# Optimization experiments

Measured on AMD Instinct MI355X. Metric: run time of the kernel, lower is better.

The kernel has to match this reference:

```python
import jax, jax.numpy as jnp
import numpy as np

N = 10000
E = 160000
B = 16
NEG_SLOPE = 0.2


def gat_conv(x, src, dst, W, a_src, a_dst, b, heads, ch):
    # x: [N, F_in]; src/dst: [E'] (self-loops included); W: [F_in, heads*ch]
    n = x.shape[0]
    h = (x @ W).reshape(n, heads, ch)                     # [N,H,C]
    alpha_src = jnp.sum(h * a_src, axis=-1)               # [N,H]
    alpha_dst = jnp.sum(h * a_dst, axis=-1)               # [N,H]
    e = jax.nn.leaky_relu(alpha_src[src] + alpha_dst[dst], NEG_SLOPE)  # [E,H]
    # segment softmax over edges grouped by destination node
    m = jax.ops.segment_max(e, dst, num_segments=n)       # [N,H]
    ex = jnp.exp(e - m[dst])                              # [E,H]
    denom = jax.ops.segment_sum(ex, dst, num_segments=n)  # [N,H]
    alpha = ex / denom[dst]                               # [E,H]
    out = jax.ops.segment_sum(alpha[:, :, None] * h[src], dst, num_segments=n)  # [N,H,C]
    return out.reshape(n, heads * ch) + b


def setup_inputs() -> dict:
    key = jax.random.key(0)
    ks = jax.random.split(key, 16)
    glorot = lambda k, shp: jax.random.normal(k, shp, jnp.float32) * np.sqrt(2.0 / (shp[0] + shp[-1]))
    inp = {
        "x": jax.random.normal(ks[0], (N, 128), jnp.float32),
        "edge_index": jax.random.randint(ks[1], (2, E), 0, N, jnp.int64),
        "batch": jnp.sort(jax.random.randint(ks[2], (N,), 0, B, jnp.int64)),
        # conv1: 128 -> 128 per head, 8 heads
        "W1": glorot(ks[3], (128, 8 * 128)),
        "att_src1": glorot(ks[4], (8, 128)),
        "att_dst1": glorot(ks[5], (8, 128)),
        "b1": jnp.zeros((8 * 128,), jnp.float32),
        # conv2: 1024 -> 64 per head, 8 heads
        "W2": glorot(ks[6], (1024, 8 * 64)),
        "att_src2": glorot(ks[7], (8, 64)),
        "att_dst2": glorot(ks[8], (8, 64)),
        "b2": jnp.zeros((8 * 64,), jnp.float32),
        "fc1_w": glorot(ks[9], (512, 32)),
        "fc1_b": jnp.zeros((32,), jnp.float32),
        "fc2_w": glorot(ks[10], (32, 10)),
        "fc2_b": jnp.zeros((10,), jnp.float32),
    }
    return inp


def reference(x, edge_index, batch, W1, att_src1, att_dst1, b1,
              W2, att_src2, att_dst2, b2, fc1_w, fc1_b, fc2_w, fc2_b):
    n = x.shape[0]
    loop = jnp.arange(n, dtype=edge_index.dtype)
    src = jnp.concatenate([edge_index[0], loop])  # PyG add_self_loops=True
    dst = jnp.concatenate([edge_index[1], loop])
    h = jax.nn.elu(gat_conv(x, src, dst, W1, att_src1, att_dst1, b1, 8, 128))   # [N,1024]
    h = jax.nn.elu(gat_conv(h, src, dst, W2, att_src2, att_dst2, b2, 8, 64))    # [N,512]
    # global mean pool over graphs
    sums = jax.ops.segment_sum(h, batch, num_segments=B)                        # [B,512]
    cnt = jax.ops.segment_sum(jnp.ones((n,), h.dtype), batch, num_segments=B)
    g = sums / jnp.maximum(cnt, 1.0)[:, None]
    g = jax.nn.elu(g @ fc1_w + fc1_b)
    return g @ fc2_w + fc2_b                                                    # [B,10]
```

## Files before the change

kernel.cpp:

```cpp
#include <hip/hip_runtime.h>
#include <math.h>

#define HEADS 8
#define NEG 0.2f

typedef unsigned short ushort_t;
typedef __attribute__((ext_vector_type(8))) short short8;
typedef float f32x4 __attribute__((ext_vector_type(4)));

__device__ inline ushort_t f2bf(float f) {
  union { float f; unsigned u; } v; v.f = f;
  unsigned r = (v.u + 0x7FFF + ((v.u >> 16) & 1)) >> 16;
  return (ushort_t)r;
}

__device__ inline float4 bf4(uint2 v) {
  union { unsigned u; float f; } a, b, c, d;
  a.u = v.x << 16; b.u = v.x & 0xffff0000u;
  c.u = v.y << 16; d.u = v.y & 0xffff0000u;
  return make_float4(a.f, b.f, c.f, d.f);
}

__device__ inline float elu_f(float v) {
  return (v > 0.f) ? v : (__expf(v) - 1.f);
}

#define GLDS16(gp, lp)                                                          \
  __builtin_amdgcn_global_load_lds(                                             \
      (const __attribute__((address_space(1))) void*)(gp),                      \
      (__attribute__((address_space(3))) void*)(lp), 16, 0, 0)

__global__ __launch_bounds__(256) void init_k(int* __restrict__ ws, int zero_words,
                                              const float* __restrict__ x,
                                              ushort_t* __restrict__ xb,
                                              const float* __restrict__ W1,
                                              ushort_t* __restrict__ w1t,
                                              const float* __restrict__ W2,
                                              ushort_t* __restrict__ w2t, int nx4) {
  __shared__ float tile[32][33];
  int blk = blockIdx.x;
  if (blk < 640) {
    const float* W; ushort_t* Wt; int K, N, tk, tn;
    if (blk < 128) { W = W1; Wt = w1t; K = 128; N = 1024; tk = blk >> 5; tn = blk & 31; }
    else { W = W2; Wt = w2t; K = 1024; N = 512; int t = blk - 128; tk = t >> 4; tn = t & 15; }
    int tx = threadIdx.x & 31, ty = threadIdx.x >> 5;
    int k0 = tk * 32, n0 = tn * 32;
#pragma unroll
    for (int r = 0; r < 4; r++)
      tile[ty + r * 8][tx] = W[(size_t)(k0 + ty + r * 8) * N + n0 + tx];
    __syncthreads();
#pragma unroll
    for (int r = 0; r < 4; r++)
      Wt[(size_t)(n0 + ty + r * 8) * K + k0 + tx] = f2bf(tile[tx][ty + r * 8]);
  } else {
    int i = (blk - 640) * 256 + threadIdx.x;
    if (i < zero_words) ws[i] = 0;
    if (i < nx4) {
      float4 v = ((const float4*)x)[i];
      ushort_t o[4] = {f2bf(v.x), f2bf(v.y), f2bf(v.z), f2bf(v.w)};
      *(uint2*)&xb[i * 4] = *(uint2*)o;
    }
  }
}

__global__ void prep_k(const int* __restrict__ ei, int* __restrict__ src,
                       int* __restrict__ dst, int* __restrict__ deg,
                       const int* __restrict__ batch, int* __restrict__ bstart,
                       int* __restrict__ bend, int E, int Nn) {
  int i = blockIdx.x * blockDim.x + threadIdx.x;
  if (i < Nn) {
    int b = batch[i];
    if (i == 0 || batch[i - 1] != b) bstart[b] = i;
    if (i == Nn - 1 || batch[i + 1] != b) bend[b] = i + 1;
  }
  if (i >= E + Nn) return;
  int s, d;
  if (i < E) { s = ei[i]; d = ei[E + i]; }
  else       { s = d = i - E; }
  src[i] = s;
  dst[i] = d;
  atomicAdd(&deg[d], 1);
}

__global__ __launch_bounds__(1024) void scan_k(const int* __restrict__ deg,
                                               int* __restrict__ offs,
                                               int* __restrict__ cursor, int Nn) {
  __shared__ int wtot[16];
  __shared__ int wexcl[16];
  __shared__ int soff_s;
  int t = threadIdx.x;
  int lane = t & 63, w = t >> 6;
  if (t == 0) soff_s = 0;
  __syncthreads();
  for (int base = 0; base < Nn; base += 4096) {
    int idx = base + 4 * t;
    int4 v = make_int4(0, 0, 0, 0);
    if (idx + 3 < Nn) v = *(const int4*)&deg[idx];
    else {
      if (idx < Nn)     v.x = deg[idx];
      if (idx + 1 < Nn) v.y = deg[idx + 1];
      if (idx + 2 < Nn) v.z = deg[idx + 2];
      if (idx + 3 < Nn) v.w = deg[idx + 3];
    }
    int s1 = v.x, s2 = s1 + v.y, s3 = s2 + v.z, s4 = s3 + v.w;
    int sc = s4;
#pragma unroll
    for (int o = 1; o < 64; o <<= 1) {
      int x = __shfl_up(sc, o);
      if (lane >= o) sc += x;
    }
    if (lane == 63) wtot[w] = sc;
    __syncthreads();
    if (w == 0) {
      int tv = (lane < 16) ? wtot[lane] : 0;
      int ts = tv;
#pragma unroll
      for (int o = 1; o < 16; o <<= 1) {
        int x = __shfl_up(ts, o);
        if (lane >= o) ts += x;
      }
      if (lane < 16) wexcl[lane] = ts - tv;
      if (lane == 15) wtot[15] = ts;
    }
    __syncthreads();
    int excl = soff_s + wexcl[w] + (sc - s4);
    int o0 = excl, o1 = excl + s1, o2 = excl + s2, o3 = excl + s3;
    if (idx < Nn)     { offs[idx] = o0;     cursor[idx] = o0; }
    if (idx + 1 < Nn) { offs[idx + 1] = o1; cursor[idx + 1] = o1; }
    if (idx + 2 < Nn) { offs[idx + 2] = o2; cursor[idx + 2] = o2; }
    if (idx + 3 < Nn) { offs[idx + 3] = o3; cursor[idx + 3] = o3; }
    int chunk_total = wtot[15];
    __syncthreads();
    if (t == 0) soff_s += chunk_total;
    __syncthreads();
  }
  if (t == 0) offs[Nn] = soff_s;
}

__global__ void scatter_k(const int* __restrict__ src, const int* __restrict__ dst,
                          int* __restrict__ cursor, int* __restrict__ psrc, int Etot) {
  int i = blockIdx.x * blockDim.x + threadIdx.x;
  if (i >= Etot) return;
  int p = atomicAdd(&cursor[dst[i]], 1);
  psrc[p] = src[i];
}

__global__ __launch_bounds__(256) void mfma_gemm_k(const ushort_t* __restrict__ A,
                                                   const ushort_t* __restrict__ Bt,
                                                   ushort_t* __restrict__ Cb,
                                                   const float* __restrict__ att_s,
                                                   const float* __restrict__ att_d,
                                                   float* __restrict__ asrc,
                                                   float* __restrict__ adst,
                                                   int M, int N, int K, int CSHIFT) {
  __shared__ __attribute__((aligned(16))) ushort_t As[128 * 64];
  __shared__ __attribute__((aligned(16))) ushort_t Bs[128 * 64];
  int tid = threadIdx.x;
  int lane = tid & 63;
  int wave = tid >> 6;
  int wm = (wave >> 1) * 64, wn = (wave & 1) * 64;
  int bm = blockIdx.y * 128, bn = blockIdx.x * 128;
  int lrow = lane & 15, lq = lane >> 4;

  f32x4 acc[4][4];
#pragma unroll
  for (int i = 0; i < 4; i++)
#pragma unroll
    for (int j = 0; j < 4; j++) acc[i][j] = 0.f;

  int srow = lane >> 3;
  int scol = 8 * ((lane & 7) ^ srow);
  const ushort_t* pa[4];
  const ushort_t* pb[4];
  ushort_t* la[4];
  ushort_t* lb[4];
#pragma unroll
  for (int c = 0; c < 4; c++) {
    int row = wave * 32 + c * 8 + srow;
    int ga = min(bm + row, M - 1);
    pa[c] = &A[(size_t)ga * K + scol];
    pb[c] = &Bt[(size_t)(bn + row) * K + scol];
    la[c] = &As[(wave * 4 + c) * 512];
    lb[c] = &Bs[(wave * 4 + c) * 512];
  }

  for (int k0 = 0; k0 < K; k0 += 64) {
    __syncthreads();
#pragma unroll
    for (int c = 0; c < 4; c++) GLDS16(pa[c] + k0, la[c]);
#pragma unroll
    for (int c = 0; c < 4; c++) GLDS16(pb[c] + k0, lb[c]);
    __syncthreads();
#pragma unroll
    for (int ks = 0; ks < 2; ks++) {
      short8 af[4], bfr[4];
#pragma unroll
      for (int t = 0; t < 4; t++) {
        int cbs = (ks * 64 + lq * 16) ^ ((lrow & 7) << 4);
        af[t]  = *(const short8*)&As[(wm + t * 16 + lrow) * 64 + (cbs >> 1)];
        bfr[t] = *(const short8*)&Bs[(wn + t * 16 + lrow) * 64 + (cbs >> 1)];
      }
#pragma unroll
      for (int i = 0; i < 4; i++)
#pragma unroll
        for (int j = 0; j < 4; j++)
          acc[i][j] = __builtin_amdgcn_mfma_f32_16x16x32_bf16(af[i], bfr[j], acc[i][j], 0, 0, 0);
    }
  }

  {
    int hh = (bn + wn) >> CSHIFT;
    float avs[4], avd[4];
#pragma unroll
    for (int j = 0; j < 4; j++) {
      int col = bn + wn + j * 16 + lrow;
      avs[j] = att_s[col];
      avd[j] = att_d[col];
    }
#pragma unroll
    for (int i = 0; i < 4; i++) {
#pragma unroll
      for (int r = 0; r < 4; r++) {
        float ps = 0.f, pd = 0.f;
#pragma unroll
        for (int j = 0; j < 4; j++) {
          float v = acc[i][j][r];
          ps += v * avs[j];
          pd += v * avd[j];
        }
#pragma unroll
        for (int o = 1; o < 16; o <<= 1) {
          ps += __shfl_xor(ps, o);
          pd += __shfl_xor(pd, o);
        }
        int row = bm + wm + i * 16 + lq * 4 + r;
        if (lrow == 0 && row < M) {
          atomicAdd(&asrc[row * HEADS + hh], ps);
          atomicAdd(&adst[row * HEADS + hh], pd);
        }
      }
    }
  }

#pragma unroll
  for (int i = 0; i < 4; i++) {
    int row0 = bm + wm + i * 16 + lq * 4;
#pragma unroll
    for (int j = 0; j < 4; j++) {
      int col = bn + wn + j * 16 + lrow;
#pragma unroll
      for (int r = 0; r < 4; r++) {
        int row = row0 + r;
        if (row < M) Cb[(size_t)row * N + col] = f2bf(acc[i][j][r]);
      }
    }
  }
}

template <int F, int CSHIFT, int BT, int NSPLIT, typename OT>
__global__ __launch_bounds__(BT) void aggregate_k(const ushort_t* __restrict__ hb,
                                                  const float* __restrict__ asrc,
                                                  const float* __restrict__ adst,
                                                  const int* __restrict__ offs,
                                                  const int* __restrict__ psrc,
                                                  const float* __restrict__ bias,
                                                  OT* __restrict__ out) {
  constexpr int CPB = F / NSPLIT;
  static_assert(CPB == 4 * BT, "CPB/thread mismatch");
  int nb = blockIdx.x;
  int n = nb / NSPLIT;
  int coff = (nb - n * NSPLIT) * CPB;
  int t = threadIdx.x;
  int c0 = coff + 4 * t;
  int hh = c0 >> CSHIFT;
  float adn = adst[n * HEADS + hh];
  int e0 = offs[n], e1 = offs[n + 1];
  float4 acc = make_float4(0.f, 0.f, 0.f, 0.f);
  float wsum = 0.f;

  int i = e0;
  int s[8];
  if (i + 8 <= e1) {
#pragma unroll
    for (int u = 0; u < 8; u++) s[u] = psrc[i + u];
  }
  while (i + 8 <= e1) {
    uint2 r[8];
    float av[8];
#pragma unroll
    for (int u = 0; u < 8; u++) r[u] = *(const uint2*)&hb[(size_t)s[u] * F + c0];
#pragma unroll
    for (int u = 0; u < 8; u++) av[u] = asrc[s[u] * HEADS + hh];
    i += 8;
    bool more = (i + 8 <= e1);
    int sn[8];
#pragma unroll
    for (int u = 0; u < 8; u++) sn[u] = more ? psrc[i + u] : 0;
#pragma unroll
    for (int u = 0; u < 8; u++) {
      float v = av[u] + adn;
      v = (v > 0.f) ? v : NEG * v;
      float w = __expf(v);
      float4 f = bf4(r[u]);
      wsum += w;
      acc.x += w * f.x;
      acc.y += w * f.y;
      acc.z += w * f.z;
      acc.w += w * f.w;
    }
#pragma unroll
    for (int u = 0; u < 8; u++) s[u] = sn[u];
  }
  for (; i < e1; i++) {
    int ss = psrc[i];
    float v = asrc[ss * HEADS + hh] + adn;
    v = (v > 0.f) ? v : NEG * v;
    float w = __expf(v);
    float4 f = bf4(*(const uint2*)&hb[(size_t)ss * F + c0]);
    wsum += w;
    acc.x += w * f.x; acc.y += w * f.y;
    acc.z += w * f.z; acc.w += w * f.w;
  }

  float inv = 1.f / wsum;
  float v0 = elu_f(acc.x * inv + bias[c0]);
  float v1 = elu_f(acc.y * inv + bias[c0 + 1]);
  float v2 = elu_f(acc.z * inv + bias[c0 + 2]);
  float v3 = elu_f(acc.w * inv + bias[c0 + 3]);
  if (sizeof(OT) == 2) {
    unsigned p0 = (unsigned)f2bf(v0) | ((unsigned)f2bf(v1) << 16);
    unsigned p1 = (unsigned)f2bf(v2) | ((unsigned)f2bf(v3) << 16);
    *(uint2*)&((ushort_t*)out)[(size_t)n * F + c0] = make_uint2(p0, p1);
  } else {
    *(float4*)&((float*)out)[(size_t)n * F + c0] = make_float4(v0, v1, v2, v3);
  }
}

__global__ __launch_bounds__(256) void pool_k(const float* __restrict__ g,
                                              const int* __restrict__ batch,
                                              float* __restrict__ sums, int Nn) {
  int c = blockIdx.x * 256 + threadIdx.x;
  int n0 = blockIdx.y * 50;
  int n1 = min(n0 + 50, Nn);
  if (n0 >= n1) return;
  float acc = 0.f;
  int cur = batch[n0];
  for (int n = n0; n < n1; n++) {
    int b = batch[n];
    if (b != cur) { atomicAdd(&sums[cur * 512 + c], acc); acc = 0.f; cur = b; }
    acc += g[(size_t)n * 512 + c];
  }
  atomicAdd(&sums[cur * 512 + c], acc);
}

__global__ __launch_bounds__(512) void mlp_k(const float* __restrict__ sums,
                                             const int* __restrict__ bstart,
                                             const int* __restrict__ bend,
                                             const float* __restrict__ w1,
                                             const float* __restrict__ b1,
                                             const float* __restrict__ w2,
                                             const float* __restrict__ b2,
                                             float* __restrict__ out) {
  __shared__ float gm[16 * 512];
  __shared__ float t1[16 * 32];
  int t = threadIdx.x;
  for (int i = t; i < 16 * 512; i += 512) {
    int b = i >> 9;
    float c = (float)(bend[b] - bstart[b]);
    gm[i] = sums[i] / fmaxf(c, 1.f);
  }
  __syncthreads();
  {
    int b = t >> 5, j = t & 31;
    float s = b1[j];
    for (int k = 0; k < 512; k++) s += gm[(b << 9) + k] * w1[k * 32 + j];
    t1[t] = elu_f(s);
  }
  __syncthreads();
  if (t < 160) {
    int b = t / 10, j = t - b * 10;
    float s = b2[j];
#pragma unroll
    for (int k = 0; k < 32; k++) s += t1[b * 32 + k] * w2[k * 10 + j];
    out[t] = s;
  }
}

extern "C" void kernel_launch(void* const* d_in, const int* in_sizes, int n_in,
                              void* d_out, int out_size, void* d_ws, size_t ws_size,
                              hipStream_t stream) {
  const float* x   = (const float*)d_in[0];
  const int*   ei  = (const int*)d_in[1];
  const int* batch = (const int*)d_in[2];
  const float* W1  = (const float*)d_in[3];
  const float* as1 = (const float*)d_in[4];
  const float* ad1 = (const float*)d_in[5];
  const float* b1  = (const float*)d_in[6];
  const float* W2  = (const float*)d_in[7];
  const float* as2 = (const float*)d_in[8];
  const float* ad2 = (const float*)d_in[9];
  const float* b2  = (const float*)d_in[10];
  const float* f1w = (const float*)d_in[11];
  const float* f1b = (const float*)d_in[12];
  const float* f2w = (const float*)d_in[13];
  const float* f2b = (const float*)d_in[14];
  float* out = (float*)d_out;

  const int Nn = in_sizes[2];
  const int E = in_sizes[1] / 2;
  const int Etot = E + Nn;

  size_t off = 0;
  auto alloc = [&](size_t elems) { size_t o = off; off += (elems + 63) & ~(size_t)63; return o; };
  int* wsi = (int*)d_ws;
  float* wsf = (float*)d_ws;

  size_t o_deg  = alloc(Nn);
  size_t o_pool = alloc(16 * 512);
  size_t o_as1  = alloc((size_t)Nn * 8);
  size_t o_ad1  = alloc((size_t)Nn * 8);
  size_t o_as2  = alloc((size_t)Nn * 8);
  size_t o_ad2  = alloc((size_t)Nn * 8);
  size_t zero_words = off;
  size_t o_bst  = alloc(64);
  size_t o_ben  = alloc(64);
  size_t o_offs = alloc(Nn + 1);
  size_t o_cur  = alloc(Nn);
  size_t o_src  = alloc(Etot);
  size_t o_dst  = alloc(Etot);
  size_t o_psrc = alloc(Etot);
  size_t o_xb   = alloc((size_t)Nn * 128 / 2);
  size_t o_w1t  = alloc(1024 * 128 / 2);
  size_t o_w2t  = alloc(512 * 1024 / 2);
  size_t o_h    = alloc((size_t)Nn * 1024 / 2);
  size_t o_g    = alloc((size_t)Nn * 1024);

  ushort_t* xb  = (ushort_t*)(wsi + o_xb);
  ushort_t* w1t = (ushort_t*)(wsi + o_w1t);
  ushort_t* w2t = (ushort_t*)(wsi + o_w2t);
  ushort_t* hb  = (ushort_t*)(wsi + o_h);
  ushort_t* g1b = (ushort_t*)(wsi + o_g);

  int eb = (Etot + 255) / 256;

  int nx4 = Nn * 128 / 4;
  int ep_work = (int)((zero_words > (size_t)nx4 ? zero_words : (size_t)nx4));
  int init_blocks = 640 + (ep_work + 255) / 256;
  init_k<<<init_blocks, 256, 0, stream>>>(wsi, (int)zero_words, x, xb,
                                          W1, w1t, W2, w2t, nx4);
  prep_k<<<eb, 256, 0, stream>>>(ei, wsi + o_src, wsi + o_dst, wsi + o_deg,
                                 batch, wsi + o_bst, wsi + o_ben, E, Nn);
  scan_k<<<1, 1024, 0, stream>>>(wsi + o_deg, wsi + o_offs, wsi + o_cur, Nn);
  scatter_k<<<eb, 256, 0, stream>>>(wsi + o_src, wsi + o_dst, wsi + o_cur,
                                    wsi + o_psrc, Etot);

  mfma_gemm_k<<<dim3(1024 / 128, (Nn + 127) / 128), 256, 0, stream>>>(
      xb, w1t, hb, as1, ad1, wsf + o_as1, wsf + o_ad1, Nn, 1024, 128, 7);
  aggregate_k<1024, 7, 128, 2, ushort_t><<<Nn * 2, 128, 0, stream>>>(
      hb, wsf + o_as1, wsf + o_ad1, wsi + o_offs, wsi + o_psrc, b1, g1b);

  mfma_gemm_k<<<dim3(512 / 128, (Nn + 127) / 128), 256, 0, stream>>>(
      g1b, w2t, hb, as2, ad2, wsf + o_as2, wsf + o_ad2, Nn, 512, 1024, 6);
  aggregate_k<512, 6, 64, 2, float><<<Nn * 2, 64, 0, stream>>>(
      hb, wsf + o_as2, wsf + o_ad2, wsi + o_offs, wsi + o_psrc, b2, wsf + o_g);

  pool_k<<<dim3(2, (Nn + 49) / 50), 256, 0, stream>>>(wsf + o_g, batch, wsf + o_pool, Nn);
  mlp_k<<<1, 512, 0, stream>>>(wsf + o_pool, wsi + o_bst, wsi + o_ben, f1w, f1b, f2w, f2b, out);
}
```

Before: 276.4 us.

## Precompute per-edge attention weights in a separate kernel before aggregation

Adds a weights_k kernel that computes exp(leaky_relu(asrc+adst)) once per edge and head, stored head-major in a workspace buffer. scatter_k now also writes the CSR-sorted destination index so this kernel can run. The aggregate kernels then read precomputed weights instead of gathering asrc and recomputing exp in every thread that shares a head. This removes redundant exp and gather work in the aggregation, at the cost of two extra launches, an extra pdst array and a write plus read of an E×8 float buffer per layer.

New measurement: 287.3 us. 3.9% more time.

```diff
diff --git a/kernel.cpp b/kernel.cpp
--- a/kernel.cpp
+++ b/kernel.cpp
@@ -138,11 +138,36 @@
 }
 
 __global__ void scatter_k(const int* __restrict__ src, const int* __restrict__ dst,
-                          int* __restrict__ cursor, int* __restrict__ psrc, int Etot) {
+                          int* __restrict__ cursor, int* __restrict__ psrc,
+                          int* __restrict__ pdst, int Etot) {
   int i = blockIdx.x * blockDim.x + threadIdx.x;
   if (i >= Etot) return;
-  int p = atomicAdd(&cursor[dst[i]], 1);
+  int d = dst[i];
+  int p = atomicAdd(&cursor[d], 1);
   psrc[p] = src[i];
+  pdst[p] = d;
+}
+
+__global__ __launch_bounds__(256) void weights_k(const int* __restrict__ psrc,
+                                                 const int* __restrict__ pdst,
+                                                 const float* __restrict__ asrc,
+                                                 const float* __restrict__ adst,
+                                                 float* __restrict__ w, int Etot) {
+  int p = blockIdx.x * 256 + threadIdx.x;
+  if (p >= Etot) return;
+  int s = psrc[p], d = pdst[p];
+  const float4* sa = (const float4*)&asrc[(size_t)s * 8];
+  const float4* da = (const float4*)&adst[(size_t)d * 8];
+  float4 s0 = sa[0], s1 = sa[1];
+  float4 d0 = da[0], d1 = da[1];
+  float vv[8] = {s0.x + d0.x, s0.y + d0.y, s0.z + d0.z, s0.w + d0.w,
+                 s1.x + d1.x, s1.y + d1.y, s1.z + d1.z, s1.w + d1.w};
+#pragma unroll
+  for (int h = 0; h < 8; h++) {
+    float v = vv[h];
+    v = (v > 0.f) ? v : NEG * v;
+    w[(size_t)h * Etot + p] = __expf(v);
+  }
 }
 
 __global__ __launch_bounds__(256) void mfma_gemm_k(const ushort_t* __restrict__ A,
@@ -259,12 +284,11 @@
 
 template <int F, int CSHIFT, int BT, int NSPLIT, typename OT>
 __global__ __launch_bounds__(BT) void aggregate_k(const ushort_t* __restrict__ hb,
-                                                  const float* __restrict__ asrc,
-                                                  const float* __restrict__ adst,
+                                                  const float* __restrict__ w,
                                                   const int* __restrict__ offs,
                                                   const int* __restrict__ psrc,
                                                   const float* __restrict__ bias,
-                                                  OT* __restrict__ out) {
+                                                  OT* __restrict__ out, int Etot) {
   constexpr int CPB = F / NSPLIT;
   static_assert(CPB == 4 * BT, "CPB/thread mismatch");
   int nb = blockIdx.x;
@@ -273,53 +297,52 @@
   int t = threadIdx.x;
   int c0 = coff + 4 * t;
   int hh = c0 >> CSHIFT;
-  float adn = adst[n * HEADS + hh];
+  const float* __restrict__ wp = w + (size_t)hh * Etot;
   int e0 = offs[n], e1 = offs[n + 1];
   float4 acc = make_float4(0.f, 0.f, 0.f, 0.f);
   float wsum = 0.f;
 
   int i = e0;
   int s[8];
+  float wv[8];
   if (i + 8 <= e1) {
 #pragma unroll
     for (int u = 0; u < 8; u++) s[u] = psrc[i + u];
+#pragma unroll
+    for (int u = 0; u < 8; u++) wv[u] = wp[i + u];
   }
   while (i + 8 <= e1) {
     uint2 r[8];
-    float av[8];
 #pragma unroll
     for (int u = 0; u < 8; u++) r[u] = *(const uint2*)&hb[(size_t)s[u] * F + c0];
-#pragma unroll
-    for (int u = 0; u < 8; u++) av[u] = asrc[s[u] * HEADS + hh];
     i += 8;
     bool more = (i + 8 <= e1);
     int sn[8];
+    float wn[8];
 #pragma unroll
     for (int u = 0; u < 8; u++) sn[u] = more ? psrc[i + u] : 0;
 #pragma unroll
+    for (int u = 0; u < 8; u++) wn[u] = more ? wp[i + u] : 0.f;
+#pragma unroll
     for (int u = 0; u < 8; u++) {
-      float v = av[u] + adn;
-      v = (v > 0.f) ? v : NEG * v;
-      float w = __expf(v);
+      float wt = wv[u];
       float4 f = bf4(r[u]);
-      wsum += w;
-      acc.x += w * f.x;
-      acc.y += w * f.y;
-      acc.z += w * f.z;
-      acc.w += w * f.w;
-    }
-#pragma unroll
-    for (int u = 0; u < 8; u++) s[u] = sn[u];
+      wsum += wt;
+      acc.x += wt * f.x;
+      acc.y += wt * f.y;
+      acc.z += wt * f.z;
+      acc.w += wt * f.w;
+    }
+#pragma unroll
+    for (int u = 0; u < 8; u++) { s[u] = sn[u]; wv[u] = wn[u]; }
   }
   for (; i < e1; i++) {
     int ss = psrc[i];
-    float v = asrc[ss * HEADS + hh] + adn;
-    v = (v > 0.f) ? v : NEG * v;
-    float w = __expf(v);
+    float wt = wp[i];
     float4 f = bf4(*(const uint2*)&hb[(size_t)ss * F + c0]);
-    wsum += w;
-    acc.x += w * f.x; acc.y += w * f.y;
-    acc.z += w * f.z; acc.w += w * f.w;
+    wsum += wt;
+    acc.x += wt * f.x; acc.y += wt * f.y;
+    acc.z += wt * f.z; acc.w += wt * f.w;
   }
 
   float inv = 1.f / wsum;
@@ -429,6 +452,8 @@
   size_t o_src  = alloc(Etot);
   size_t o_dst  = alloc(Etot);
   size_t o_psrc = alloc(Etot);
+  size_t o_pdst = alloc(Etot);
+  size_t o_w    = alloc((size_t)Etot * 8);
   size_t o_xb   = alloc((size_t)Nn * 128 / 2);
   size_t o_w1t  = alloc(1024 * 128 / 2);
   size_t o_w2t  = alloc(512 * 1024 / 2);
@@ -452,17 +477,21 @@
                                  batch, wsi + o_bst, wsi + o_ben, E, Nn);
   scan_k<<<1, 1024, 0, stream>>>(wsi + o_deg, wsi + o_offs, wsi + o_cur, Nn);
   scatter_k<<<eb, 256, 0, stream>>>(wsi + o_src, wsi + o_dst, wsi + o_cur,
-                                    wsi + o_psrc, Etot);
+                                    wsi + o_psrc, wsi + o_pdst, Etot);
 
   mfma_gemm_k<<<dim3(1024 / 128, (Nn + 127) / 128), 256, 0, stream>>>(
       xb, w1t, hb, as1, ad1, wsf + o_as1, wsf + o_ad1, Nn, 1024, 128, 7);
+  weights_k<<<eb, 256, 0, stream>>>(wsi + o_psrc, wsi + o_pdst,
+                                    wsf + o_as1, wsf + o_ad1, wsf + o_w, Etot);
   aggregate_k<1024, 7, 128, 2, ushort_t><<<Nn * 2, 128, 0, stream>>>(
-      hb, wsf + o_as1, wsf + o_ad1, wsi + o_offs, wsi + o_psrc, b1, g1b);
+      hb, wsf + o_w, wsi + o_offs, wsi + o_psrc, b1, g1b, Etot);
 
   mfma_gemm_k<<<dim3(512 / 128, (Nn + 127) / 128), 256, 0, stream>>>(
       g1b, w2t, hb, as2, ad2, wsf + o_as2, wsf + o_ad2, Nn, 512, 1024, 6);
+  weights_k<<<eb, 256, 0, stream>>>(wsi + o_psrc, wsi + o_pdst,
+                                    wsf + o_as2, wsf + o_ad2, wsf + o_w, Etot);
   aggregate_k<512, 6, 64, 2, float><<<Nn * 2, 64, 0, stream>>>(
-      hb, wsf + o_as2, wsf + o_ad2, wsi + o_offs, wsi + o_psrc, b2, wsf + o_g);
+      hb, wsf + o_w, wsi + o_offs, wsi + o_psrc, b2, wsf + o_g, Etot);
 
   pool_k<<<dim3(2, (Nn + 49) / 50), 256, 0, stream>>>(wsf + o_g, batch, wsf + o_pool, Nn);
   mlp_k<<<1, 512, 0, stream>>>(wsf + o_pool, wsi + o_bst, wsi + o_ben, f1w, f1b, f2w, f2b, out);
```

## Double-buffer LDS tiles in MFMA GEMM to overlap global loads with compute

Applied to the files above, without the earlier changes.

Doubles the shared-memory A/B tiles and restructures the K loop so the next tile is staged via direct global-to-LDS loads while MFMAs run on the current buffer. A single waitcnt plus barrier per iteration replaces the two __syncthreads. This is meant to hide global load latency behind compute. In exchange, LDS use doubles to 64KB per block, which may reduce occupancy.

Result: no change. 279.4 us (+1.1%).

```diff
diff --git a/kernel.cpp b/kernel.cpp
--- a/kernel.cpp
+++ b/kernel.cpp
@@ -153,8 +153,8 @@
                                                    float* __restrict__ asrc,
                                                    float* __restrict__ adst,
                                                    int M, int N, int K, int CSHIFT) {
-  __shared__ __attribute__((aligned(16))) ushort_t As[128 * 64];
-  __shared__ __attribute__((aligned(16))) ushort_t Bs[128 * 64];
+  __shared__ __attribute__((aligned(16))) ushort_t As[2][128 * 64];
+  __shared__ __attribute__((aligned(16))) ushort_t Bs[2][128 * 64];
   int tid = threadIdx.x;
   int lane = tid & 63;
   int wave = tid >> 6;
@@ -172,33 +172,32 @@
   int scol = 8 * ((lane & 7) ^ srow);
   const ushort_t* pa[4];
   const ushort_t* pb[4];
-  ushort_t* la[4];
-  ushort_t* lb[4];
+  int lofs[4];
 #pragma unroll
   for (int c = 0; c < 4; c++) {
     int row = wave * 32 + c * 8 + srow;
     int ga = min(bm + row, M - 1);
     pa[c] = &A[(size_t)ga * K + scol];
     pb[c] = &Bt[(size_t)(bn + row) * K + scol];
-    la[c] = &As[(wave * 4 + c) * 512];
-    lb[c] = &Bs[(wave * 4 + c) * 512];
-  }
-
-  for (int k0 = 0; k0 < K; k0 += 64) {
-    __syncthreads();
-#pragma unroll
-    for (int c = 0; c < 4; c++) GLDS16(pa[c] + k0, la[c]);
-#pragma unroll
-    for (int c = 0; c < 4; c++) GLDS16(pb[c] + k0, lb[c]);
-    __syncthreads();
+    lofs[c] = (wave * 4 + c) * 512;
+  }
+
+  auto stage = [&](int buf, int k0) {
+#pragma unroll
+    for (int c = 0; c < 4; c++) GLDS16(pa[c] + k0, &As[buf][lofs[c]]);
+#pragma unroll
+    for (int c = 0; c < 4; c++) GLDS16(pb[c] + k0, &Bs[buf][lofs[c]]);
+  };
+
+  auto compute = [&](int buf) {
 #pragma unroll
     for (int ks = 0; ks < 2; ks++) {
       short8 af[4], bfr[4];
 #pragma unroll
       for (int t = 0; t < 4; t++) {
         int cbs = (ks * 64 + lq * 16) ^ ((lrow & 7) << 4);
-        af[t]  = *(const short8*)&As[(wm + t * 16 + lrow) * 64 + (cbs >> 1)];
-        bfr[t] = *(const short8*)&Bs[(wn + t * 16 + lrow) * 64 + (cbs >> 1)];
+        af[t]  = *(const short8*)&As[buf][(wm + t * 16 + lrow) * 64 + (cbs >> 1)];
+        bfr[t] = *(const short8*)&Bs[buf][(wn + t * 16 + lrow) * 64 + (cbs >> 1)];
       }
 #pragma unroll
       for (int i = 0; i < 4; i++)
@@ -206,7 +205,21 @@
         for (int j = 0; j < 4; j++)
           acc[i][j] = __builtin_amdgcn_mfma_f32_16x16x32_bf16(af[i], bfr[j], acc[i][j], 0, 0, 0);
     }
-  }
+  };
+
+  int NT = K >> 6;
+  stage(0, 0);
+  asm volatile("s_waitcnt vmcnt(0)" ::: "memory");
+  __builtin_amdgcn_s_barrier();
+  int cur = 0;
+  for (int t = 0; t + 1 < NT; ++t) {
+    stage(cur ^ 1, (t + 1) << 6);
+    compute(cur);
+    asm volatile("s_waitcnt vmcnt(0)" ::: "memory");
+    __builtin_amdgcn_s_barrier();
+    cur ^= 1;
+  }
+  compute(cur);
 
   {
     int hh = (bn + wn) >> CSHIFT;
```
